# Kernel optimization log

Measured on AMD Instinct MI355X. Metric: run time of the kernel, lower is better.

The kernel has to match this reference:

```python
import jax, jax.numpy as jnp
import numpy as np

DIM = 96; K = 3; DIL = 1
UF = K + DIL * (K - 1)   # unfoldSize = 5
PAD = UF // 2            # reflection pad = 2


def conv2d(x, w, b=None, pad=0, dil=1, groups=1):
    y = jax.lax.conv_general_dilated(
        x, w, (1, 1), [(pad, pad), (pad, pad)], rhs_dilation=(dil, dil),
        dimension_numbers=('NCHW', 'OIHW', 'NCHW'), feature_group_count=groups)
    if b is not None:
        y = y + b[None, :, None, None]
    return y


def group_norm(x, s, b, groups, eps=1e-5):
    n, c, h, w = x.shape
    xg = x.reshape(n, groups, -1)
    m = xg.mean(-1, keepdims=True)
    v = xg.var(-1, keepdims=True)
    xg = (xg - m) * jax.lax.rsqrt(v + eps)
    return xg.reshape(n, c, h, w) * s[None, :, None, None] + b[None, :, None, None]


def prelu(x, a):
    return jnp.where(x >= 0, x, a[0] * x)


def setup_inputs() -> dict:
    key = jax.random.key(0)
    ks = jax.random.split(key, 16)
    d = DIM; dq = d // 4
    rn = lambda i, shape, sc: jax.random.normal(ks[i], shape, jnp.float32) * sc
    return {
        'x': jax.random.normal(ks[0], (8, d, 128, 128), jnp.float32),
        'cf_w': rn(1, (d * K * K, d, 1, 1), 0.1),
        'gnf_s': jnp.ones((d * K * K,)), 'gnf_b': jnp.zeros((d * K * K,)),
        'lb1_w': rn(2, (dq, d, 1, 1), 0.1), 'lb1_b': jnp.zeros((dq,)), 'pr1': jnp.full((1,), 0.25),
        'lbd1_w': rn(3, (dq, 1, 3, 3), 0.2), 'lbd1_b': jnp.zeros((dq,)),
        'lb2_w': rn(4, (dq, dq, 1, 1), 0.2), 'lb2_b': jnp.zeros((dq,)), 'pr2': jnp.full((1,), 0.25),
        'lbd2_w': rn(5, (dq, 1, 3, 3), 0.2), 'lbd2_b': jnp.zeros((dq,)),
        'lb3_w': rn(6, (dq, dq, 1, 1), 0.2), 'lb3_b': jnp.zeros((dq,)), 'pr3': jnp.full((1,), 0.25),
        'lbd3_w': rn(7, (dq, 1, 3, 3), 0.2), 'lbd3_b': jnp.zeros((dq,)),
        'lb4_w': rn(8, (dq, dq, 1, 1), 0.2), 'lb4_b': jnp.zeros((dq,)), 'pr4': jnp.full((1,), 0.25),
        'lb5_w': rn(9, (d, dq, 1, 1), 0.2), 'lb5_b': jnp.zeros((d,)),
        'gnh_s': jnp.ones((d,)), 'gnh_b': jnp.zeros((d,)),
        'hb_w': rn(10, (d, d, 3, 3), 0.05), 'hb_b': jnp.zeros((d,)),
        'ff1_w': rn(11, (2 * d, 2 * d, 1, 1), 0.07), 'ff1_b': jnp.zeros((2 * d,)),
        'gnff_s': jnp.ones((2 * d,)), 'gnff_b': jnp.zeros((2 * d,)),
        'ff2_w': rn(12, (d, 2 * d, 1, 1), 0.07), 'ff2_b': jnp.zeros((d,)),
    }


def reference(x, cf_w, gnf_s, gnf_b, lb1_w, lb1_b, pr1, lbd1_w, lbd1_b,
              lb2_w, lb2_b, pr2, lbd2_w, lbd2_b, lb3_w, lb3_b, pr3,
              lbd3_w, lbd3_b, lb4_w, lb4_b, pr4, lb5_w, lb5_b,
              gnh_s, gnh_b, hb_w, hb_b, ff1_w, ff1_b, gnff_s, gnff_b,
              ff2_w, ff2_b):
    n, c, h, w = x.shape
    d = DIM; dq = d // 4
    # --- dynamic filter from global average pool ---
    fi = x.mean((2, 3), keepdims=True)                 # (n, d, 1, 1)
    fw = conv2d(fi, cf_w)                              # (n, d*9, 1, 1)
    fw = group_norm(fw, gnf_s, gnf_b, 4)
    fw = jax.nn.softmax(fw.reshape(n, d, K * K), axis=-1)  # (n, d, 9)
    # --- masked unfold (involution gather): only offsets on the (DIL+1)-stride grid ---
    xp = jnp.pad(x, ((0, 0), (0, 0), (PAD, PAD), (PAD, PAD)), mode='reflect')
    offs = [(i, j) for i in range(0, UF, DIL + 1) for j in range(0, UF, DIL + 1)]
    patches = jnp.stack([xp[:, :, i:i + h, j:j + w] for i, j in offs], axis=2)  # (n,d,9,h,w)
    low = jnp.einsum('nckhw,nck->nchw', patches, fw)
    high = x - low
    # --- low-frequency multi-dilation branch ---
    y = prelu(conv2d(low, lb1_w, lb1_b), pr1)
    y = conv2d(y, lbd1_w, lbd1_b, pad=5, dil=5, groups=dq)
    y = prelu(conv2d(y, lb2_w, lb2_b), pr2)
    y = conv2d(y, lbd2_w, lbd2_b, pad=1, groups=dq)
    y = prelu(conv2d(y, lb3_w, lb3_b), pr3)
    y = conv2d(y, lbd3_w, lbd3_b, pad=3, dil=3, groups=dq)
    y = prelu(conv2d(y, lb4_w, lb4_b), pr4)
    enh_low = conv2d(y, lb5_w, lb5_b)
    # --- high-frequency branch (GN -> LeakyReLU -> 3x3) + residual ---
    hh = group_norm(high, gnh_s, gnh_b, 4)
    hh = jnp.where(hh >= 0, hh, 0.01 * hh)
    enh_high = conv2d(hh, hb_w, hb_b, pad=1) + high
    # --- frequency fusion ---
    f = jnp.concatenate([enh_low, enh_high], axis=1)
    f = conv2d(f, ff1_w, ff1_b)
    f = group_norm(f, gnff_s, gnff_b, 4)
    f = jax.nn.gelu(f, approximate=False)
    return conv2d(f, ff2_w, ff2_b)
```

## Files before the change

### kernel.cpp

```cpp
#include <hip/hip_runtime.h>
#include <math.h>

#define HW 16384
#define WIDTH 128

typedef short bf16x8 __attribute__((ext_vector_type(8)));
typedef float f32x4 __attribute__((ext_vector_type(4)));
typedef unsigned short ushort8 __attribute__((ext_vector_type(8)));
typedef unsigned short ushort4v __attribute__((ext_vector_type(4)));
typedef unsigned short ushort2v __attribute__((ext_vector_type(2)));

__device__ __forceinline__ float wave_sum(float v) {
#pragma unroll
  for (int o = 32; o > 0; o >>= 1) v += __shfl_down(v, o, 64);
  return v;
}

__device__ __forceinline__ unsigned short f2bf(float f) {
  unsigned u = __float_as_uint(f);
  return (unsigned short)((u + 0x7fffu + ((u >> 16) & 1u)) >> 16);
}

__device__ __forceinline__ float bf2f(unsigned short s) {
  return __uint_as_float((unsigned)s << 16);
}

__device__ __forceinline__ float gelu_exact(float z) {
  float u = z * 0.70710678118654752f;
  float ax = fabsf(u);
  float t = __builtin_amdgcn_rcpf(fmaf(0.3275911f, ax, 1.0f));
  float poly = t * fmaf(t, fmaf(t, fmaf(t, fmaf(t, 1.061405429f, -1.453152027f),
                                        1.421413741f), -0.284496736f), 0.254829592f);
  float e = __expf(-ax * ax);
  float erf_abs = fmaf(-poly, e, 1.0f);
  float erf = copysignf(erf_abs, z);
  return 0.5f * z * (1.0f + erf);
}

__global__ __launch_bounds__(256) void k_mean(const float* __restrict__ x,
                                              float* __restrict__ fi) {
  __shared__ float sm[4];
  int nc = blockIdx.x;
  const float4* p = (const float4*)(x + (size_t)nc * HW);
  float s = 0.f;
  for (int i = threadIdx.x; i < HW / 4; i += 256) {
    float4 v = p[i];
    s += (v.x + v.y) + (v.z + v.w);
  }
  s = wave_sum(s);
  int wid = threadIdx.x >> 6, lane = threadIdx.x & 63;
  if (!lane) sm[wid] = s;
  __syncthreads();
  if (!threadIdx.x) fi[nc] = (sm[0] + sm[1] + sm[2] + sm[3]) * (1.f / 16384.f);
}

__global__ __launch_bounds__(256) void k_filter(const float* __restrict__ fi,
                                                const float* __restrict__ cf_w,
                                                const float* __restrict__ gnf_s,
                                                const float* __restrict__ gnf_b,
                                                float* __restrict__ filt) {
  int n = blockIdx.x;
  int t = threadIdx.x;
  __shared__ __align__(16) float sfi[96];
  __shared__ float sfw[864];
  __shared__ float gstat[8];
  if (t < 96) sfi[t] = fi[n * 96 + t];
  __syncthreads();
  for (int oc = t; oc < 864; oc += 256) {
    const float4* wr = (const float4*)(cf_w + (size_t)oc * 96);
    const float4* fr = (const float4*)sfi;
    float a = 0.f;
#pragma unroll
    for (int q = 0; q < 24; q++) {
      float4 w4 = wr[q];
      float4 f4 = fr[q];
      a += w4.x * f4.x + w4.y * f4.y + w4.z * f4.z + w4.w * f4.w;
    }
    sfw[oc] = a;
  }
  __syncthreads();
  if (t < 4) {
    float s = 0.f, ss = 0.f;
    for (int i = 0; i < 216; i++) {
      float v = sfw[t * 216 + i];
      s += v;
      ss += v * v;
    }
    float m = s * (1.f / 216.f);
    float var = ss * (1.f / 216.f) - m * m;
    gstat[t * 2] = m;
    gstat[t * 2 + 1] = rsqrtf(var + 1e-5f);
  }
  __syncthreads();
  for (int oc = t; oc < 864; oc += 256) {
    int g = oc / 216;
    sfw[oc] = (sfw[oc] - gstat[g * 2]) * gstat[g * 2 + 1] * gnf_s[oc] + gnf_b[oc];
  }
  __syncthreads();
  if (t < 96) {
    float v[9], mx = -1e30f;
#pragma unroll
    for (int k = 0; k < 9; k++) {
      v[k] = sfw[t * 9 + k];
      mx = fmaxf(mx, v[k]);
    }
    float s = 0.f;
#pragma unroll
    for (int k = 0; k < 9; k++) {
      v[k] = expf(v[k] - mx);
      s += v[k];
    }
    float inv = 1.f / s;
#pragma unroll
    for (int k = 0; k < 9; k++) filt[((size_t)n * 96 + t) * 9 + k] = v[k] * inv;
  }
}

__global__ __launch_bounds__(256) void k_invol(const float* __restrict__ x,
                                               const float* __restrict__ filt,
                                               float* __restrict__ low,
                                               float* __restrict__ high) {
  int nc = blockIdx.y;
  const float* xp = x + (size_t)nc * HW;
  const float* fp = filt + (size_t)nc * 9;
  float f[9];
#pragma unroll
  for (int k = 0; k < 9; k++) f[k] = fp[k];
  int idx = blockIdx.x * 256 + threadIdx.x;
  int y = idx >> 7, xx = idx & 127;
  int ry[3], rx[3];
#pragma unroll
  for (int d = 0; d < 3; d++) {
    int p = y + 2 * d - 2;
    if (p < 0) p = -p;
    if (p > 127) p = 254 - p;
    ry[d] = p;
    int q = xx + 2 * d - 2;
    if (q < 0) q = -q;
    if (q > 127) q = 254 - q;
    rx[d] = q;
  }
  float acc = 0.f;
#pragma unroll
  for (int i = 0; i < 3; i++)
#pragma unroll
    for (int j = 0; j < 3; j++) acc = fmaf(f[i * 3 + j], xp[ry[i] * WIDTH + rx[j]], acc);
  float xv = xp[idx];
  size_t o = (size_t)nc * HW + idx;
  low[o] = acc;
  high[o] = xv - acc;
}

template <int CIN, int COUT, bool PRELU>
__global__ __launch_bounds__(256) void k_conv1x1(const float* __restrict__ in,
                                                 const float* __restrict__ w,
                                                 const float* __restrict__ b,
                                                 const float* __restrict__ pr,
                                                 float* __restrict__ out) {
  int n = blockIdx.y;
  int pix = blockIdx.x * 256 + threadIdx.x;
  const float* ip = in + (size_t)n * CIN * HW + pix;
  float acc[COUT];
#pragma unroll
  for (int o = 0; o < COUT; o++) acc[o] = b[o];
  for (int c = 0; c < CIN; c += 4) {
    float v0 = ip[(size_t)c * HW];
    float v1 = ip[(size_t)(c + 1) * HW];
    float v2 = ip[(size_t)(c + 2) * HW];
    float v3 = ip[(size_t)(c + 3) * HW];
#pragma unroll
    for (int o = 0; o < COUT; o++) {
      float4 wv = *(const float4*)(w + (size_t)o * CIN + c);
      acc[o] = fmaf(v0, wv.x, acc[o]);
      acc[o] = fmaf(v1, wv.y, acc[o]);
      acc[o] = fmaf(v2, wv.z, acc[o]);
      acc[o] = fmaf(v3, wv.w, acc[o]);
    }
  }
  float a = PRELU ? pr[0] : 0.f;
  float* op = out + (size_t)n * COUT * HW + pix;
#pragma unroll
  for (int o = 0; o < COUT; o++) {
    float v = acc[o];
    if (PRELU) v = v >= 0.f ? v : a * v;
    op[(size_t)o * HW] = v;
  }
}

template <int DILA>
__global__ __launch_bounds__(256) void k_dwfuse(const float* __restrict__ in,
                                                const float* __restrict__ dw,
                                                const float* __restrict__ dwb,
                                                const float* __restrict__ w1,
                                                const float* __restrict__ b1,
                                                const float* __restrict__ pr,
                                                float* __restrict__ out) {
  int n = blockIdx.y;
  int pix = blockIdx.x * 256 + threadIdx.x;
  int y = pix >> 7, xx = pix & 127;
  const float* ip = in + (size_t)n * 24 * HW;
  float acc[24];
#pragma unroll
  for (int o = 0; o < 24; o++) acc[o] = b1[o];
  for (int c = 0; c < 24; c += 4) {
    float d[4];
#pragma unroll
    for (int q = 0; q < 4; q++) {
      float a = dwb[c + q];
      const float* cp = ip + (size_t)(c + q) * HW;
#pragma unroll
      for (int i = 0; i < 3; i++) {
        int yy = y + DILA * (i - 1);
        if (yy < 0 || yy >= 128) continue;
#pragma unroll
        for (int j = 0; j < 3; j++) {
          int xj = xx + DILA * (j - 1);
          if (xj < 0 || xj >= 128) continue;
          a = fmaf(dw[(c + q) * 9 + i * 3 + j], cp[yy * WIDTH + xj], a);
        }
      }
      d[q] = a;
    }
#pragma unroll
    for (int o = 0; o < 24; o++) {
      float4 wv = *(const float4*)(w1 + (size_t)o * 24 + c);
      acc[o] = fmaf(d[0], wv.x, acc[o]);
      acc[o] = fmaf(d[1], wv.y, acc[o]);
      acc[o] = fmaf(d[2], wv.z, acc[o]);
      acc[o] = fmaf(d[3], wv.w, acc[o]);
    }
  }
  float a = pr[0];
  float* op = out + (size_t)n * 24 * HW + pix;
#pragma unroll
  for (int o = 0; o < 24; o++) {
    float v = acc[o];
    op[(size_t)o * HW] = v >= 0.f ? v : a * v;
  }
}

__global__ __launch_bounds__(256) void k_lb5(const float* __restrict__ in,
                                             const float* __restrict__ w,
                                             const float* __restrict__ b,
                                             unsigned short* __restrict__ out) {
  int n = blockIdx.y;
  int pix = blockIdx.x * 256 + threadIdx.x;
  const float* ip = in + (size_t)n * 24 * HW + pix;
  float acc[96];
#pragma unroll
  for (int o = 0; o < 96; o++) acc[o] = b[o];
  for (int c = 0; c < 24; c += 4) {
    float v0 = ip[(size_t)c * HW];
    float v1 = ip[(size_t)(c + 1) * HW];
    float v2 = ip[(size_t)(c + 2) * HW];
    float v3 = ip[(size_t)(c + 3) * HW];
#pragma unroll
    for (int o = 0; o < 96; o++) {
      float4 wv = *(const float4*)(w + (size_t)o * 24 + c);
      acc[o] = fmaf(v0, wv.x, acc[o]);
      acc[o] = fmaf(v1, wv.y, acc[o]);
      acc[o] = fmaf(v2, wv.z, acc[o]);
      acc[o] = fmaf(v3, wv.w, acc[o]);
    }
  }
  unsigned short* op = out + ((size_t)n * HW + pix) * 96;
#pragma unroll
  for (int c8 = 0; c8 < 12; c8++) {
    ushort8 pk;
#pragma unroll
    for (int j = 0; j < 8; j++) pk[j] = f2bf(acc[c8 * 8 + j]);
    *(ushort8*)&op[c8 * 8] = pk;
  }
}

__global__ __launch_bounds__(256) void k_gnhigh_part(const float* __restrict__ h,
                                                     float* __restrict__ stats) {
  int ng = blockIdx.x;
  const float4* p = (const float4*)(h + (size_t)ng * 393216 + (size_t)blockIdx.y * 49152);
  float s = 0.f, ss = 0.f;
  for (int i = threadIdx.x; i < 12288; i += 256) {
    float4 v = p[i];
    s += (v.x + v.y) + (v.z + v.w);
    ss += (v.x * v.x + v.y * v.y) + (v.z * v.z + v.w * v.w);
  }
  s = wave_sum(s);
  ss = wave_sum(ss);
  __shared__ float sm[8];
  int wid = threadIdx.x >> 6, lane = threadIdx.x & 63;
  if (!lane) {
    sm[wid] = s;
    sm[4 + wid] = ss;
  }
  __syncthreads();
  if (!threadIdx.x) {
    atomicAdd(&stats[ng * 2], sm[0] + sm[1] + sm[2] + sm[3]);
    atomicAdd(&stats[ng * 2 + 1], sm[4] + sm[5] + sm[6] + sm[7]);
  }
}

__global__ void k_gnfin(float* stats, float inv_cnt) {
  int i = threadIdx.x;
  float s = stats[i * 2], ss = stats[i * 2 + 1];
  float m = s * inv_cnt;
  float var = ss * inv_cnt - m * m;
  stats[i * 2] = m;
  stats[i * 2 + 1] = rsqrtf(var + 1e-5f);
}

__global__ __launch_bounds__(256) void k_prep_hn(const float* __restrict__ high,
                                                 const float* __restrict__ hstats,
                                                 const float* __restrict__ gs,
                                                 const float* __restrict__ gb,
                                                 unsigned short* __restrict__ hn) {
  __shared__ unsigned short sm[64 * 104];
  int n = blockIdx.y;
  int px0 = blockIdx.x * 64;
  int t = threadIdx.x;
  int px = t & 63, cg = t >> 6;
  float hm[4], hi[4];
#pragma unroll
  for (int g = 0; g < 4; g++) {
    hm[g] = hstats[(n * 4 + g) * 2];
    hi[g] = hstats[(n * 4 + g) * 2 + 1];
  }
#pragma unroll
  for (int c0 = 0; c0 < 96; c0 += 8) {
    int c = c0 + cg * 2;
    int g = c / 24;
    float v0 = high[((size_t)(n * 96 + c)) * HW + px0 + px];
    float v1 = high[((size_t)(n * 96 + c + 1)) * HW + px0 + px];
    float h0 = (v0 - hm[g]) * hi[g] * gs[c] + gb[c];
    float h1 = (v1 - hm[g]) * hi[g] * gs[c + 1] + gb[c + 1];
    h0 = h0 >= 0.f ? h0 : 0.01f * h0;
    h1 = h1 >= 0.f ? h1 : 0.01f * h1;
    ushort2v p;
    p.x = f2bf(h0);
    p.y = f2bf(h1);
    *(ushort2v*)&sm[px * 104 + c] = p;
  }
  __syncthreads();
#pragma unroll
  for (int k = 0; k < 3; k++) {
    int idx = t + k * 256;
    int p = idx / 12, c8 = idx % 12;
    ushort8 v = *(ushort8*)&sm[p * 104 + c8 * 8];
    *(ushort8*)&hn[((size_t)n * HW + px0 + p) * 96 + c8 * 8] = v;
  }
}

__global__ __launch_bounds__(256) void k_prep_w(const float* __restrict__ w,
                                                unsigned short* __restrict__ wbf) {
  int i = blockIdx.x * 256 + threadIdx.x;
  int tap = i / 9216;
  int r = i - tap * 9216;
  int oc = r / 96, cin = r - oc * 96;
  wbf[i] = f2bf(w[(size_t)(oc * 96 + cin) * 9 + tap]);
}

__global__ __launch_bounds__(256) void k_prep_ffw(const float* __restrict__ w1,
                                                  const float* __restrict__ w2,
                                                  unsigned short* __restrict__ o1,
                                                  unsigned short* __restrict__ o2) {
  int i = blockIdx.x * 256 + threadIdx.x;
  if (i < 36864)
    o1[i] = f2bf(w1[i]);
  else
    o2[i - 36864] = f2bf(w2[i - 36864]);
}

__global__ __launch_bounds__(256) void k_hbconv_mfma(const unsigned short* __restrict__ hn,
                                                     const unsigned short* __restrict__ wbf,
                                                     const float* __restrict__ bias,
                                                     const float* __restrict__ high,
                                                     unsigned short* __restrict__ ehigh) {
  __shared__ __align__(16) unsigned short stile[6 * 34 * 104];
  int t = threadIdx.x;
  int n = blockIdx.z;
  int x0 = blockIdx.x * 32, y0 = blockIdx.y * 4;
  for (int idx = t; idx < 2448; idx += 256) {
    int p = idx / 12, c8 = idx % 12;
    int ly = p / 34, lx = p - ly * 34;
    int gy = y0 + ly - 1, gx = x0 + lx - 1;
    ushort8 v = (ushort8)0;
    if ((unsigned)gy < 128u && (unsigned)gx < 128u)
      v = *(const ushort8*)&hn[((size_t)n * HW + gy * 128 + gx) * 96 + c8 * 8];
    *(ushort8*)&stile[(ly * 34 + lx) * 104 + c8 * 8] = v;
  }
  __syncthreads();
  int wv = t >> 6;
  int lane = t & 63;
  int l15 = lane & 15, l4 = lane >> 4;
  f32x4 acc[6][2];
#pragma unroll
  for (int mf = 0; mf < 6; mf++)
#pragma unroll
    for (int nf = 0; nf < 2; nf++) acc[mf][nf] = (f32x4)0.f;
#pragma unroll 1
  for (int tap = 0; tap < 9; tap++) {
    int ky = tap / 3, kx = tap - ky * 3;
    const unsigned short* wt = wbf + (size_t)tap * 9216;
#pragma unroll
    for (int kk = 0; kk < 3; kk++) {
      bf16x8 a[6], b[2];
#pragma unroll
      for (int mf = 0; mf < 6; mf++)
        a[mf] = *(const bf16x8*)&wt[(mf * 16 + l15) * 96 + kk * 32 + l4 * 8];
#pragma unroll
      for (int nf = 0; nf < 2; nf++) {
        int p = (wv + ky) * 34 + (nf * 16 + l15 + kx);
        b[nf] = *(const bf16x8*)&stile[p * 104 + kk * 32 + l4 * 8];
      }
#pragma unroll
      for (int mf = 0; mf < 6; mf++)
#pragma unroll
        for (int nf = 0; nf < 2; nf++)
          acc[mf][nf] = __builtin_amdgcn_mfma_f32_16x16x32_bf16(a[mf], b[nf], acc[mf][nf], 0, 0, 0);
    }
  }
  int gy = y0 + wv;
  unsigned short* sT = stile;
  __syncthreads();
#pragma unroll
  for (int mf = 0; mf < 6; mf++) {
#pragma unroll
    for (int nf = 0; nf < 2; nf++) {
      int lx = nf * 16 + l15;
      int p = wv * 32 + lx;
      ushort4v pk;
#pragma unroll
      for (int r = 0; r < 4; r++) {
        int oc = mf * 16 + l4 * 4 + r;
        size_t o = ((size_t)(n * 96 + oc)) * HW + gy * 128 + x0 + lx;
        float v = acc[mf][nf][r] + bias[oc] + high[o];
        pk[r] = f2bf(v);
      }
      *(ushort4v*)&sT[p * 104 + mf * 16 + l4 * 4] = pk;
    }
  }
  __syncthreads();
  for (int idx = t; idx < 1536; idx += 256) {
    int p = idx / 12, c8 = idx % 12;
    int py = p >> 5, lx = p & 31;
    size_t gpx = (size_t)n * HW + (y0 + py) * 128 + x0 + lx;
    *(ushort8*)&ehigh[gpx * 96 + c8 * 8] = *(ushort8*)&sT[p * 104 + c8 * 8];
  }
}

__global__ __launch_bounds__(256) void k_ff1_mfma(const unsigned short* __restrict__ elow,
                                                  const unsigned short* __restrict__ ehigh,
                                                  const unsigned short* __restrict__ wbf,
                                                  const float* __restrict__ bias,
                                                  unsigned short* __restrict__ tbf,
                                                  float* __restrict__ ffstats) {
  __shared__ __align__(16) unsigned short sB[64 * 200];
  __shared__ float sred[4][8];
  int t = threadIdx.x;
  size_t pxbase = (size_t)blockIdx.x * 64;
  int n = blockIdx.x >> 8;
  for (int idx = t; idx < 1536; idx += 256) {
    int p = idx / 24, c8 = idx % 24;
    ushort8 v = (c8 < 12) ? *(const ushort8*)&elow[(pxbase + p) * 96 + c8 * 8]
                          : *(const ushort8*)&ehigh[(pxbase + p) * 96 + (c8 - 12) * 8];
    *(ushort8*)&sB[p * 200 + c8 * 8] = v;
  }
  __syncthreads();
  int wv = t >> 6, lane = t & 63, l15 = lane & 15, l4 = lane >> 4;
  f32x4 acc[12];
#pragma unroll
  for (int mf = 0; mf < 12; mf++) acc[mf] = (f32x4)0.f;
  const unsigned short* wp = wbf + l15 * 192 + l4 * 8;
  const unsigned short* bp = &sB[(wv * 16 + l15) * 200 + l4 * 8];
#pragma unroll
  for (int kk = 0; kk < 6; kk++) {
    bf16x8 b = *(const bf16x8*)(bp + kk * 32);
#pragma unroll
    for (int mf = 0; mf < 12; mf++) {
      bf16x8 a = *(const bf16x8*)(wp + mf * 3072 + kk * 32);
      acc[mf] = __builtin_amdgcn_mfma_f32_16x16x32_bf16(a, b, acc[mf], 0, 0, 0);
    }
  }
  float s[4] = {0.f, 0.f, 0.f, 0.f}, ss[4] = {0.f, 0.f, 0.f, 0.f};
#pragma unroll
  for (int mf = 0; mf < 12; mf++) {
    int g = mf / 3;
    ushort4v pk;
#pragma unroll
    for (int r = 0; r < 4; r++) {
      float v = acc[mf][r] + bias[mf * 16 + l4 * 4 + r];
      s[g] += v;
      ss[g] += v * v;
      pk[r] = f2bf(v);
    }
    *(ushort4v*)&sB[(wv * 16 + l15) * 200 + mf * 16 + l4 * 4] = pk;
  }
#pragma unroll
  for (int g = 0; g < 4; g++) {
    s[g] = wave_sum(s[g]);
    ss[g] = wave_sum(ss[g]);
  }
  if (!lane) {
#pragma unroll
    for (int g = 0; g < 4; g++) {
      sred[wv][g] = s[g];
      sred[wv][4 + g] = ss[g];
    }
  }
  __syncthreads();
  for (int idx = t; idx < 1536; idx += 256) {
    int p = idx / 24, c8 = idx % 24;
    *(ushort8*)&tbf[(pxbase + p) * 192 + c8 * 8] = *(ushort8*)&sB[p * 200 + c8 * 8];
  }
  if (t < 8) {
    float tot = sred[0][t] + sred[1][t] + sred[2][t] + sred[3][t];
    atomicAdd(&ffstats[(n * 4 + (t & 3)) * 2 + (t >> 2)], tot);
  }
}

__global__ __launch_bounds__(256) void k_ff2_mfma(const unsigned short* __restrict__ tbf,
                                                  const float* __restrict__ ffstats,
                                                  const float* __restrict__ gs,
                                                  const float* __restrict__ gb,
                                                  const unsigned short* __restrict__ wbf,
                                                  const float* __restrict__ bias,
                                                  float* __restrict__ out) {
  __shared__ __align__(16) unsigned short sB[64 * 200];
  int t = threadIdx.x;
  size_t pxbase = (size_t)blockIdx.x * 64;
  int n = blockIdx.x >> 8;
  float fm[4], fvv[4];
#pragma unroll
  for (int g = 0; g < 4; g++) {
    fm[g] = ffstats[(n * 4 + g) * 2];
    fvv[g] = ffstats[(n * 4 + g) * 2 + 1];
  }
  ushort8 raw[6];
  int pp[6], cc[6];
#pragma unroll
  for (int k = 0; k < 6; k++) {
    int idx = t + k * 256;
    int p = idx / 24, c8 = idx - p * 24;
    pp[k] = p;
    cc[k] = c8 * 8;
    raw[k] = *(const ushort8*)&tbf[(pxbase + p) * 192 + cc[k]];
  }
#pragma unroll
  for (int k = 0; k < 6; k++) {
    int c = cc[k], g = c / 48;
    ushort8 pk;
#pragma unroll
    for (int j = 0; j < 8; j++) {
      float rv = bf2f(raw[k][j]);
      float z = (rv - fm[g]) * fvv[g] * gs[c + j] + gb[c + j];
      pk[j] = f2bf(gelu_exact(z));
    }
    *(ushort8*)&sB[pp[k] * 200 + c] = pk;
  }
  __syncthreads();
  int wv = t >> 6, lane = t & 63, l15 = lane & 15, l4 = lane >> 4;
  f32x4 acc[6];
#pragma unroll
  for (int mf = 0; mf < 6; mf++) acc[mf] = (f32x4)0.f;
  const unsigned short* wp = wbf + l15 * 192 + l4 * 8;
  const unsigned short* bp = &sB[(wv * 16 + l15) * 200 + l4 * 8];
#pragma unroll
  for (int kk = 0; kk < 6; kk++) {
    bf16x8 b = *(const bf16x8*)(bp + kk * 32);
#pragma unroll
    for (int mf = 0; mf < 6; mf++) {
      bf16x8 a = *(const bf16x8*)(wp + mf * 3072 + kk * 32);
      acc[mf] = __builtin_amdgcn_mfma_f32_16x16x32_bf16(a, b, acc[mf], 0, 0, 0);
    }
  }
  int lpx = (blockIdx.x & 255) * 64 + wv * 16 + l15;
#pragma unroll
  for (int mf = 0; mf < 6; mf++) {
#pragma unroll
    for (int r = 0; r < 4; r++) {
      int oc = mf * 16 + l4 * 4 + r;
      out[((size_t)(n * 96 + oc)) * HW + lpx] = acc[mf][r] + bias[oc];
    }
  }
}

extern "C" void kernel_launch(void* const* d_in, const int* in_sizes, int n_in,
                              void* d_out, int out_size, void* d_ws, size_t ws_size,
                              hipStream_t stream) {
  const float* x = (const float*)d_in[0];
  const float* cf_w = (const float*)d_in[1];
  const float* gnf_s = (const float*)d_in[2];
  const float* gnf_b = (const float*)d_in[3];
  const float* lb1_w = (const float*)d_in[4];
  const float* lb1_b = (const float*)d_in[5];
  const float* pr1 = (const float*)d_in[6];
  const float* lbd1_w = (const float*)d_in[7];
  const float* lbd1_b = (const float*)d_in[8];
  const float* lb2_w = (const float*)d_in[9];
  const float* lb2_b = (const float*)d_in[10];
  const float* pr2 = (const float*)d_in[11];
  const float* lbd2_w = (const float*)d_in[12];
  const float* lbd2_b = (const float*)d_in[13];
  const float* lb3_w = (const float*)d_in[14];
  const float* lb3_b = (const float*)d_in[15];
  const float* pr3 = (const float*)d_in[16];
  const float* lbd3_w = (const float*)d_in[17];
  const float* lbd3_b = (const float*)d_in[18];
  const float* lb4_w = (const float*)d_in[19];
  const float* lb4_b = (const float*)d_in[20];
  const float* pr4 = (const float*)d_in[21];
  const float* lb5_w = (const float*)d_in[22];
  const float* lb5_b = (const float*)d_in[23];
  const float* gnh_s = (const float*)d_in[24];
  const float* gnh_b = (const float*)d_in[25];
  const float* hb_w = (const float*)d_in[26];
  const float* hb_b = (const float*)d_in[27];
  const float* ff1_w = (const float*)d_in[28];
  const float* ff1_b = (const float*)d_in[29];
  const float* gnff_s = (const float*)d_in[30];
  const float* gnff_b = (const float*)d_in[31];
  const float* ff2_w = (const float*)d_in[32];
  const float* ff2_b = (const float*)d_in[33];

  const size_t SPC = (size_t)8 * 96 * HW;
  const size_t YSZ = (size_t)8 * 24 * HW;
  float* ws = (float*)d_ws;
  float* buf_low = ws;
  unsigned short* buf_tbf = (unsigned short*)ws;
  float* buf_high = ws + SPC;
  unsigned short* buf_hn = (unsigned short*)(ws + 2 * SPC);
  unsigned short* buf_ehigh = (unsigned short*)(ws + 2 * SPC + SPC / 2);
  unsigned short* buf_elow = (unsigned short*)(ws + 3 * SPC);
  unsigned short* buf_wbf = (unsigned short*)(ws + 3 * SPC + SPC / 2);
  unsigned short* buf_wff1 = buf_wbf + 82944;
  unsigned short* buf_wff2 = buf_wff1 + 36864;
  float* buf_y1 = ws + 4 * SPC;
  float* buf_y2 = buf_y1 + YSZ;
  float* buf_fi = buf_y2 + YSZ;
  float* buf_filt = buf_fi + 768;
  float* buf_hst = buf_filt + 6912;
  float* buf_ffst = buf_hst + 64;

  hipMemsetAsync(buf_hst, 0, 128 * sizeof(float), stream);

  k_mean<<<768, 256, 0, stream>>>(x, buf_fi);
  k_filter<<<8, 256, 0, stream>>>(buf_fi, cf_w, gnf_s, gnf_b, buf_filt);
  k_invol<<<dim3(64, 768), 256, 0, stream>>>(x, buf_filt, buf_low, buf_high);

  k_conv1x1<96, 24, true><<<dim3(64, 8), 256, 0, stream>>>(buf_low, lb1_w, lb1_b, pr1, buf_y1);
  k_dwfuse<5><<<dim3(64, 8), 256, 0, stream>>>(buf_y1, lbd1_w, lbd1_b, lb2_w, lb2_b, pr2,
                                               buf_y2);
  k_dwfuse<1><<<dim3(64, 8), 256, 0, stream>>>(buf_y2, lbd2_w, lbd2_b, lb3_w, lb3_b, pr3,
                                               buf_y1);
  k_dwfuse<3><<<dim3(64, 8), 256, 0, stream>>>(buf_y1, lbd3_w, lbd3_b, lb4_w, lb4_b, pr4,
                                               buf_y2);
  k_lb5<<<dim3(64, 8), 256, 0, stream>>>(buf_y2, lb5_w, lb5_b, buf_elow);

  k_gnhigh_part<<<dim3(32, 8), 256, 0, stream>>>(buf_high, buf_hst);
  k_gnfin<<<1, 32, 0, stream>>>(buf_hst, 1.f / 393216.f);
  k_prep_w<<<324, 256, 0, stream>>>(hb_w, buf_wbf);
  k_prep_ffw<<<216, 256, 0, stream>>>(ff1_w, ff2_w, buf_wff1, buf_wff2);
  k_prep_hn<<<dim3(256, 8), 256, 0, stream>>>(buf_high, buf_hst, gnh_s, gnh_b, buf_hn);
  k_hbconv_mfma<<<dim3(4, 32, 8), 256, 0, stream>>>(buf_hn, buf_wbf, hb_b, buf_high, buf_ehigh);

  k_ff1_mfma<<<2048, 256, 0, stream>>>(buf_elow, buf_ehigh, buf_wff1, ff1_b, buf_tbf, buf_ffst);
  k_gnfin<<<1, 32, 0, stream>>>(buf_ffst, 1.f / 786432.f);
  k_ff2_mfma<<<2048, 256, 0, stream>>>(buf_tbf, buf_ffst, gnff_s, gnff_b, buf_wff2, ff2_b,
                                       (float*)d_out);
}
```

Measured before the change: 689.2 us.

## Split FF1/FF2 MFMA work by output channels, keep weights in registers

```diff
diff --git a/kernel.cpp b/kernel.cpp
--- a/kernel.cpp
+++ b/kernel.cpp
@@ -453,7 +453,6 @@
                                                   unsigned short* __restrict__ tbf,
                                                   float* __restrict__ ffstats) {
   __shared__ __align__(16) unsigned short sB[64 * 200];
-  __shared__ float sred[4][8];
   int t = threadIdx.x;
   size_t pxbase = (size_t)blockIdx.x * 64;
   int n = blockIdx.x >> 8;
@@ -463,56 +462,59 @@
                           : *(const ushort8*)&ehigh[(pxbase + p) * 96 + (c8 - 12) * 8];
     *(ushort8*)&sB[p * 200 + c8 * 8] = v;
   }
-  __syncthreads();
   int wv = t >> 6, lane = t & 63, l15 = lane & 15, l4 = lane >> 4;
-  f32x4 acc[12];
-#pragma unroll
-  for (int mf = 0; mf < 12; mf++) acc[mf] = (f32x4)0.f;
-  const unsigned short* wp = wbf + l15 * 192 + l4 * 8;
-  const unsigned short* bp = &sB[(wv * 16 + l15) * 200 + l4 * 8];
+  const unsigned short* wp = wbf + (size_t)(wv * 48 + l15) * 192 + l4 * 8;
+  bf16x8 aw[3][6];
+#pragma unroll
+  for (int mf = 0; mf < 3; mf++)
+#pragma unroll
+    for (int kk = 0; kk < 6; kk++)
+      aw[mf][kk] = *(const bf16x8*)(wp + mf * 3072 + kk * 32);
+  __syncthreads();
+  f32x4 acc[3][4];
+#pragma unroll
+  for (int mf = 0; mf < 3; mf++)
+#pragma unroll
+    for (int nf = 0; nf < 4; nf++) acc[mf][nf] = (f32x4)0.f;
 #pragma unroll
   for (int kk = 0; kk < 6; kk++) {
-    bf16x8 b = *(const bf16x8*)(bp + kk * 32);
-#pragma unroll
-    for (int mf = 0; mf < 12; mf++) {
-      bf16x8 a = *(const bf16x8*)(wp + mf * 3072 + kk * 32);
-      acc[mf] = __builtin_amdgcn_mfma_f32_16x16x32_bf16(a, b, acc[mf], 0, 0, 0);
-    }
-  }
-  float s[4] = {0.f, 0.f, 0.f, 0.f}, ss[4] = {0.f, 0.f, 0.f, 0.f};
-#pragma unroll
-  for (int mf = 0; mf < 12; mf++) {
-    int g = mf / 3;
-    ushort4v pk;
-#pragma unroll
-    for (int r = 0; r < 4; r++) {
-      float v = acc[mf][r] + bias[mf * 16 + l4 * 4 + r];
-      s[g] += v;
-      ss[g] += v * v;
-      pk[r] = f2bf(v);
-    }
-    *(ushort4v*)&sB[(wv * 16 + l15) * 200 + mf * 16 + l4 * 4] = pk;
-  }
-#pragma unroll
-  for (int g = 0; g < 4; g++) {
-    s[g] = wave_sum(s[g]);
-    ss[g] = wave_sum(ss[g]);
-  }
+    bf16x8 b[4];
+#pragma unroll
+    for (int nf = 0; nf < 4; nf++)
+      b[nf] = *(const bf16x8*)&sB[(nf * 16 + l15) * 200 + kk * 32 + l4 * 8];
+#pragma unroll
+    for (int mf = 0; mf < 3; mf++)
+#pragma unroll
+      for (int nf = 0; nf < 4; nf++)
+        acc[mf][nf] = __builtin_amdgcn_mfma_f32_16x16x32_bf16(aw[mf][kk], b[nf], acc[mf][nf], 0, 0, 0);
+  }
+  __syncthreads();
+  float s = 0.f, ss = 0.f;
+#pragma unroll
+  for (int mf = 0; mf < 3; mf++) {
+#pragma unroll
+    for (int nf = 0; nf < 4; nf++) {
+      ushort4v pk;
+#pragma unroll
+      for (int r = 0; r < 4; r++) {
+        float v = acc[mf][nf][r] + bias[wv * 48 + mf * 16 + l4 * 4 + r];
+        s += v;
+        ss += v * v;
+        pk[r] = f2bf(v);
+      }
+      *(ushort4v*)&sB[(nf * 16 + l15) * 200 + wv * 48 + mf * 16 + l4 * 4] = pk;
+    }
+  }
+  s = wave_sum(s);
+  ss = wave_sum(ss);
   if (!lane) {
-#pragma unroll
-    for (int g = 0; g < 4; g++) {
-      sred[wv][g] = s[g];
-      sred[wv][4 + g] = ss[g];
-    }
+    atomicAdd(&ffstats[(n * 4 + wv) * 2 + 0], s);
+    atomicAdd(&ffstats[(n * 4 + wv) * 2 + 1], ss);
   }
   __syncthreads();
   for (int idx = t; idx < 1536; idx += 256) {
     int p = idx / 24, c8 = idx % 24;
     *(ushort8*)&tbf[(pxbase + p) * 192 + c8 * 8] = *(ushort8*)&sB[p * 200 + c8 * 8];
-  }
-  if (t < 8) {
-    float tot = sred[0][t] + sred[1][t] + sred[2][t] + sred[3][t];
-    atomicAdd(&ffstats[(n * 4 + (t & 3)) * 2 + (t >> 2)], tot);
   }
 }
 
@@ -543,6 +545,14 @@
     cc[k] = c8 * 8;
     raw[k] = *(const ushort8*)&tbf[(pxbase + p) * 192 + cc[k]];
   }
+  int wv = t >> 6, lane = t & 63, l15 = lane & 15, l4 = lane >> 4;
+  const unsigned short* wp = wbf + (size_t)((wv & 1) * 48 + l15) * 192 + l4 * 8;
+  bf16x8 aw[3][6];
+#pragma unroll
+  for (int mf = 0; mf < 3; mf++)
+#pragma unroll
+    for (int kk = 0; kk < 6; kk++)
+      aw[mf][kk] = *(const bf16x8*)(wp + mf * 3072 + kk * 32);
 #pragma unroll
   for (int k = 0; k < 6; k++) {
     int c = cc[k], g = c / 48;
@@ -556,28 +566,34 @@
     *(ushort8*)&sB[pp[k] * 200 + c] = pk;
   }
   __syncthreads();
-  int wv = t >> 6, lane = t & 63, l15 = lane & 15, l4 = lane >> 4;
-  f32x4 acc[6];
-#pragma unroll
-  for (int mf = 0; mf < 6; mf++) acc[mf] = (f32x4)0.f;
-  const unsigned short* wp = wbf + l15 * 192 + l4 * 8;
-  const unsigned short* bp = &sB[(wv * 16 + l15) * 200 + l4 * 8];
+  f32x4 acc[3][2];
+#pragma unroll
+  for (int mf = 0; mf < 3; mf++)
+#pragma unroll
+    for (int nf = 0; nf < 2; nf++) acc[mf][nf] = (f32x4)0.f;
+  int pxh = (wv >> 1) * 32;
 #pragma unroll
   for (int kk = 0; kk < 6; kk++) {
-    bf16x8 b = *(const bf16x8*)(bp + kk * 32);
-#pragma unroll
-    for (int mf = 0; mf < 6; mf++) {
-      bf16x8 a = *(const bf16x8*)(wp + mf * 3072 + kk * 32);
-      acc[mf] = __builtin_amdgcn_mfma_f32_16x16x32_bf16(a, b, acc[mf], 0, 0, 0);
-    }
-  }
-  int lpx = (blockIdx.x & 255) * 64 + wv * 16 + l15;
-#pragma unroll
-  for (int mf = 0; mf < 6; mf++) {
-#pragma unroll
-    for (int r = 0; r < 4; r++) {
-      int oc = mf * 16 + l4 * 4 + r;
-      out[((size_t)(n * 96 + oc)) * HW + lpx] = acc[mf][r] + bias[oc];
+    bf16x8 b[2];
+#pragma unroll
+    for (int nf = 0; nf < 2; nf++)
+      b[nf] = *(const bf16x8*)&sB[(pxh + nf * 16 + l15) * 200 + kk * 32 + l4 * 8];
+#pragma unroll
+    for (int mf = 0; mf < 3; mf++)
+#pragma unroll
+      for (int nf = 0; nf < 2; nf++)
+        acc[mf][nf] = __builtin_amdgcn_mfma_f32_16x16x32_bf16(aw[mf][kk], b[nf], acc[mf][nf], 0, 0, 0);
+  }
+  int lpx0 = (blockIdx.x & 255) * 64 + pxh + l15;
+#pragma unroll
+  for (int mf = 0; mf < 3; mf++) {
+#pragma unroll
+    for (int nf = 0; nf < 2; nf++) {
+#pragma unroll
+      for (int r = 0; r < 4; r++) {
+        int oc = (wv & 1) * 48 + mf * 16 + l4 * 4 + r;
+        out[((size_t)(n * 96 + oc)) * HW + lpx0 + nf * 16] = acc[mf][nf][r] + bias[oc];
+      }
     }
   }
 }
```

After: 753.5 us. 9.3% more time.
